# Performance work log

Measured on AMD Instinct MI355X. Metric: run time of the kernel, lower is better.

## Reference

```python
import jax, jax.numpy as jnp
import numpy as np

# Dimensions (production-scale, see shape_source)
B, L, D = 16, 64, 256      # batch, text length, char_emb
U = 500                    # number of distinct units (characters/phonemes)
V = 10000                  # vocab size
MIN_WL, MAX_WL = 4, 10     # min/max extracted word length
WL = MAX_WL - MIN_WL + 1   # number of candidate word lengths (7)
TEMP = 0.1                 # g.temperature
INS_COST = 1.0             # per-character insertion/deletion cost


def setup_inputs() -> dict:
    key = jax.random.key(0)
    k1, k2, k3, k4 = jax.random.split(key, 4)
    word_repr = jax.random.normal(k1, (B, L, D), jnp.float32)
    unit_repr = jax.random.normal(k2, (U, D), jnp.float32)
    indexed_segments = jax.random.randint(k3, (V, MAX_WL), 0, U)
    vocab_length = jax.random.randint(k4, (V,), MIN_WL, MAX_WL + 1)
    return {
        "word_repr": word_repr,
        "unit_repr": unit_repr,
        "indexed_segments": indexed_segments,
        "vocab_length": vocab_length,
    }


def _soft_max(x, axis):
    w = jnp.exp(jax.nn.log_softmax(x / TEMP, axis=axis))
    value = (x * w).sum(axis)
    index = jnp.argmax(x, axis=axis)
    return value, index


def _soft_min(x, axis):
    w = jnp.exp(jax.nn.log_softmax(-x / TEMP, axis=axis))
    value = (x * w).sum(axis)
    index = jnp.argmin(x, axis=axis)
    return value, index


def _soft_threshold(x):
    return (jax.nn.celu(1.0 - 2.0 * x) + 1.0) / 2.0


def reference(word_repr, unit_repr, indexed_segments, vocab_length):
    # --- cosine char-similarity between text positions and vocab units ---
    wn = word_repr / jnp.linalg.norm(word_repr, axis=-1, keepdims=True)   # (B,L,D)
    un = unit_repr / jnp.linalg.norm(unit_repr, axis=-1, keepdims=True)   # (U,D)
    sim = jnp.einsum('bld,ud->blu', wn, un)                               # (B,L,U)
    # pad along length so s+j gathers are in-range; padded dist is masked later
    simp = jnp.pad(sim, ((0, 0), (0, MAX_WL), (0, 0)))                    # (B,L+ML,U)

    wls = jnp.arange(MIN_WL, MAX_WL + 1)                                  # (WL,)

    # --- aligned edit-distance accumulation d(v, w) over char positions ---
    # ed[b,s,k,v] = sum_{j < min(wl_k, len_v)} (1 - cos(text[b,s+j], vocab_char[v,j]))
    ed = jnp.zeros((B, L, WL, V), jnp.float32)
    for j in range(MAX_WL):
        d_j = 1.0 - simp[:, j:j + L, :][:, :, indexed_segments[:, j]]     # (B,L,V)
        m_j = (j < jnp.minimum(wls[:, None], vocab_length[None, :]))      # (WL,V)
        ed = ed + d_j[:, :, None, :] * m_j.astype(jnp.float32)[None, None]
    # length-mismatch penalty (insert/delete)
    ed = ed + INS_COST * jnp.abs(wls[:, None] - vocab_length[None, :]).astype(jnp.float32)

    # --- soft-min over vocab: matched_ed_dist / matched_vocab ---
    matched_ed, matched_vocab = _soft_min(ed, axis=-1)                    # (B,L,WL)
    matched_length = vocab_length[matched_vocab]                          # (B,L,WL)
    # soft threshold on per-character distance, then score = thresh * |w|
    matched_thresh = _soft_threshold(matched_ed / wls.astype(jnp.float32))
    matched_score = matched_thresh * wls.astype(jnp.float32)              # (B,L,WL)

    # --- viability and scatter restore into dense (batch, len_s, len_e) ---
    s_idx = jnp.arange(L)[:, None]                                        # (L,1)
    viable = (s_idx + wls[None, :]) <= L                                  # (L,WL)
    score = jnp.where(viable[None], matched_score, 0.0)                   # (B,L,WL)
    e_idx = jnp.clip(s_idx + wls[None, :] - 1, 0, L - 1)                  # (L,WL)
    s_grid = jnp.broadcast_to(s_idx, (L, WL))
    dense = jnp.zeros((B, L, L), jnp.float32).at[:, s_grid, e_idx].add(
        score * viable[None].astype(jnp.float32))                         # (B,len_s,len_e)

    # --- soft-max over all candidate spans ---
    flat = dense.reshape(B, L * L)
    best_score, best_idx = _soft_max(flat, axis=-1)                       # (B,)
    start = best_idx // L
    end = best_idx % L
    wl_sel = jnp.clip(end - start + 1 - MIN_WL, 0, WL - 1)
    best_vocab = matched_vocab[jnp.arange(B), start, wl_sel]              # (B,)

    return start, end, best_score, best_vocab, dense
```

## Files before the change

### kernel.cpp

```cpp
#include <hip/hip_runtime.h>

#define NB 16
#define NL 64
#define ND 256
#define NU 500
#define NV 10000
#define MINWL 4
#define MAXWL 10
#define NWL 7
#define ITEMP 10.0f
#define L2I 14.4269504088896f
#define NT 512

__global__ __launch_bounds__(512) void k_sort(const int* __restrict__ vlen,
                                              int* __restrict__ origv,
                                              int* __restrict__ bases) {
    int t = threadIdx.x;
    const int CH = 20;
    int lo = t * CH, hi = min(lo + CH, NV);
    unsigned long long hA = 0, hB = 0;
    for (int v = lo; v < hi; ++v) {
        int l = vlen[v] - MINWL;
        int sh = (l & 3) * 16;
        unsigned long long inc = 1ULL << sh;
        bool isA = l < 4;
        hA += isA ? inc : 0ULL;
        hB += isA ? 0ULL : inc;
    }
    int lane = t & 63, wv = t >> 6;
    unsigned long long iA = hA, iB = hB;
#pragma unroll
    for (int o = 1; o < 64; o <<= 1) {
        unsigned long long a2 = (unsigned long long)__shfl_up((long long)iA, o);
        unsigned long long b2 = (unsigned long long)__shfl_up((long long)iB, o);
        if (lane >= o) { iA += a2; iB += b2; }
    }
    __shared__ unsigned long long wA[8], wB[8];
    __shared__ int base_s[8];
    if (lane == 63) { wA[wv] = iA; wB[wv] = iB; }
    __syncthreads();
    unsigned long long pA = 0, pB = 0, tA = 0, tB = 0;
#pragma unroll
    for (int w2 = 0; w2 < 8; ++w2) {
        if (w2 < wv) { pA += wA[w2]; pB += wB[w2]; }
        tA += wA[w2]; tB += wB[w2];
    }
    unsigned long long eA = pA + iA - hA, eB = pB + iB - hB;
    if (t == 0) {
        int tot[7] = {(int)(tA & 0xFFFF), (int)((tA >> 16) & 0xFFFF),
                      (int)((tA >> 32) & 0xFFFF), (int)((tA >> 48) & 0xFFFF),
                      (int)(tB & 0xFFFF), (int)((tB >> 16) & 0xFFFF),
                      (int)((tB >> 32) & 0xFFFF)};
        int run = 0;
        for (int l = 0; l < 7; ++l) { base_s[l] = run; bases[l] = run; run += tot[l]; }
        base_s[7] = run; bases[7] = run;
    }
    __syncthreads();
    unsigned long long qA = eA + ((unsigned long long)base_s[0] |
                                  ((unsigned long long)base_s[1] << 16) |
                                  ((unsigned long long)base_s[2] << 32) |
                                  ((unsigned long long)base_s[3] << 48));
    unsigned long long qB = eB + ((unsigned long long)base_s[4] |
                                  ((unsigned long long)base_s[5] << 16) |
                                  ((unsigned long long)base_s[6] << 32));
    for (int v = lo; v < hi; ++v) {
        int l = vlen[v] - MINWL;
        int sh = (l & 3) * 16;
        bool isA = l < 4;
        unsigned long long cur = isA ? qA : qB;
        int pos = (int)((cur >> sh) & 0xFFFF);
        origv[pos] = v;
        unsigned long long inc = 1ULL << sh;
        qA += isA ? inc : 0ULL;
        qB += isA ? 0ULL : inc;
    }
}

__global__ __launch_bounds__(256) void k_gather(const int* __restrict__ origv,
                                                const int* __restrict__ seg,
                                                int* __restrict__ segT) {
    int i = blockIdx.x * 256 + threadIdx.x;
    if (i >= NV) return;
    int v = origv[i];
    const int2* sp = (const int2*)(seg + v * MAXWL);
#pragma unroll
    for (int jj = 0; jj < 5; ++jj) {
        int2 p = sp[jj];
        segT[(2 * jj) * NV + i] = p.x;
        segT[(2 * jj + 1) * NV + i] = p.y;
    }
}

#define SSTR 260
#define SIM_LDS_BYTES ((2 * 32 * SSTR + 64) * 4)

__global__ __launch_bounds__(256) void k_sim(const float* __restrict__ word,
                                             const float* __restrict__ unit,
                                             float* __restrict__ sim) {
    extern __shared__ float lds[];
    float* wt = lds;
    float* ut = lds + 32 * SSTR;
    float* scaleW = lds + 64 * SSTR;
    float* scaleU = scaleW + 32;
    int blk = blockIdx.x;
    int uc = blk & 15, lt = (blk >> 4) & 1, b = blk >> 5;
    int l0 = lt * 32, u0 = uc * 32;
    int t = threadIdx.x;

#pragma unroll
    for (int i = 0; i < 32; ++i)
        wt[i * SSTR + t] = word[(b * NL + l0 + i) * ND + t];
#pragma unroll
    for (int i = 0; i < 32; ++i) {
        int u = u0 + i;
        ut[i * SSTR + t] = (u < NU) ? unit[u * ND + t] : 1.0f;
    }
    __syncthreads();
#pragma unroll
    for (int h = 0; h < 2; ++h) {
        int r = (t >> 4) + h * 16, p = t & 15;
        float sw = 0.f, su = 0.f;
#pragma unroll
        for (int c = 0; c < 16; ++c) {
            float x = wt[r * SSTR + p * 16 + c];
            float y = ut[r * SSTR + p * 16 + c];
            sw += x * x; su += y * y;
        }
#pragma unroll
        for (int o = 1; o < 16; o <<= 1) {
            sw += __shfl_xor(sw, o);
            su += __shfl_xor(su, o);
        }
        if (p == 0) { scaleW[r] = 1.0f / sqrtf(sw); scaleU[r] = 1.0f / sqrtf(su); }
    }
    __syncthreads();

    int lane = t & 15;
    int lp = t >> 4;
    int l = lp * 2;
    const float4* w0p = (const float4*)(wt + l * SSTR);
    const float4* w1p = (const float4*)(wt + (l + 1) * SSTR);
    const float4* x0p = (const float4*)(ut + lane * SSTR);
    const float4* x1p = (const float4*)(ut + (lane + 16) * SSTR);
    float a00 = 0.f, a01 = 0.f, a10 = 0.f, a11 = 0.f;
#pragma unroll 8
    for (int dq = 0; dq < ND / 4; ++dq) {
        float4 w0 = w0p[dq], w1 = w1p[dq], x0 = x0p[dq], x1 = x1p[dq];
        a00 += w0.x * x0.x + w0.y * x0.y + w0.z * x0.z + w0.w * x0.w;
        a01 += w0.x * x1.x + w0.y * x1.y + w0.z * x1.z + w0.w * x1.w;
        a10 += w1.x * x0.x + w1.y * x0.y + w1.z * x0.z + w1.w * x0.w;
        a11 += w1.x * x1.x + w1.y * x1.y + w1.z * x1.z + w1.w * x1.w;
    }
    float sw0 = scaleW[l], sw1 = scaleW[l + 1];
    float su0 = scaleU[lane], su1 = scaleU[lane + 16];
    int gu0 = u0 + lane, gu1 = u0 + lane + 16;
    int base = (b * NL + l0 + l) * NU;
    if (gu0 < NU) { sim[base + gu0] = a00 * (sw0 * su0); sim[base + NU + gu0] = a10 * (sw1 * su0); }
    if (gu1 < NU) { sim[base + gu1] = a01 * (sw0 * su1); sim[base + NU + gu1] = a11 * (sw1 * su1); }
}


template <int CTRL, int RM, bool BC>
__device__ __forceinline__ void red_step(float& m, int& ix, float& S, float& W) {
    float tm = __int_as_float(__builtin_amdgcn_update_dpp(
        __float_as_int(m), __float_as_int(m), CTRL, RM, 0xF, false));
    int ti = __builtin_amdgcn_update_dpp(ix, ix, CTRL, RM, 0xF, false);
    float tS = __int_as_float(__builtin_amdgcn_update_dpp(
        0, __float_as_int(S), CTRL, RM, 0xF, BC));
    float tW = __int_as_float(__builtin_amdgcn_update_dpp(
        0, __float_as_int(W), CTRL, RM, 0xF, BC));
    bool take = (tm < m) || (tm == m && ti < ix);
    ix = take ? ti : ix;
    m = take ? tm : m;
    S += tS;
    W += tW;
}

template <int L>
__device__ __forceinline__ void bucket_pass(int lo, int hi, int t, int wlmax, int kmax,
                                            const int* __restrict__ segT,
                                            const float* __restrict__ dl,
                                            float* m, float* S, float* W, int* ix) {
    if (L - 5 > kmax) return;
    float Sb = 0.f, Wb = 0.f, Sm = 0.f, Wm = 0.f;
    float mb = 3.0e38f, mm = 3.0e38f;
    int ixb = 0, ixm = 0;
    for (int i0 = lo; i0 < hi; i0 += NT) {
        int i = i0 + t;
        bool valid = i < hi;
        int ic = valid ? i : hi - 1;
        float d[L];
#pragma unroll
        for (int j = 0; j < L; ++j) {
            float g = dl[j * NU + segT[j * NV + ic]];
            d[j] = (j < 4) ? g : ((j < wlmax) ? g : 0.0f);
        }
        d[0] = valid ? d[0] : 3.0e38f;
        float q = ((d[0] + d[1]) + d[2]) + d[3];
        float pm = q;
#pragma unroll
        for (int j = 4; j < L; ++j) {
            if (j == L - 1) pm = q;
            q += d[j];
        }
        float wb = __builtin_amdgcn_exp2f(fmaf(q, -L2I, (float)L * L2I));
        Sb += wb;
        Wb = fmaf(q, wb, Wb);
        bool ltb = q < mb;
        ixb = ltb ? i : ixb;
        mb = ltb ? q : mb;
        if constexpr (L >= 5) {
            float edm = pm + 1.0f;
            float wm_ = __builtin_amdgcn_exp2f(fmaf(edm, -L2I, (float)(L - 1) * L2I));
            Sm += wm_;
            Wm = fmaf(edm, wm_, Wm);
            bool ltm = edm < mm;
            ixm = ltm ? i : ixm;
            mm = ltm ? edm : mm;
        }
    }
#pragma unroll
    for (int k = 0; k < NWL; ++k) {
        if (k >= L - 4) {
            if (k <= kmax) {
                float c = (float)(k + 4 - L);
                S[k] += Sb;
                W[k] += fmaf(c, Sb, Wb);
                float cand = mb + c;
                bool take = (cand < m[k]) || (cand == m[k] && ixb < ix[k]);
                ix[k] = take ? ixb : ix[k];
                m[k] = take ? cand : m[k];
            }
        }
        if constexpr (L >= 5) {
            if (k == L - 5 && k <= kmax) {
                S[k] += Sm;
                W[k] += Wm;
                bool take = (mm < m[k]) || (mm == m[k] && ixm < ix[k]);
                ix[k] = take ? ixm : ix[k];
                m[k] = take ? mm : m[k];
            }
        }
    }
}

__global__ __launch_bounds__(NT, 4) void k_extract(const float* __restrict__ sim,
                                                   const int* __restrict__ segT,
                                                   const int* __restrict__ origv,
                                                   const int* __restrict__ basesG,
                                                   float* __restrict__ dense,
                                                   int* __restrict__ mv) {
    int blk = blockIdx.x;
    int s = blk & (NL - 1), b = blk >> 6;
    int t = threadIdx.x;
    int wlmax = min(MAXWL, NL - s);
    if (wlmax < MINWL) {
        if (t < NL) dense[blk * NL + t] = 0.0f;
        return;
    }
    int kmax = wlmax - MINWL;

    int bs[8];
#pragma unroll
    for (int i = 0; i < 8; ++i) bs[i] = __builtin_amdgcn_readfirstlane(basesG[i]);

    __shared__ float dl[MAXWL * NU];
    for (int j = 0; j < wlmax; ++j)
        if (t < NU) dl[j * NU + t] = 1.0f - sim[(b * NL + s + j) * NU + t];
    __syncthreads();

    float m[NWL], S[NWL], W[NWL];
    int ix[NWL];
#pragma unroll
    for (int k = 0; k < NWL; ++k) { m[k] = 3.0e38f; S[k] = 0.f; W[k] = 0.f; ix[k] = 0; }

    bucket_pass<4>(bs[0], bs[1], t, wlmax, kmax, segT, dl, m, S, W, ix);
    bucket_pass<5>(bs[1], bs[2], t, wlmax, kmax, segT, dl, m, S, W, ix);
    bucket_pass<6>(bs[2], bs[3], t, wlmax, kmax, segT, dl, m, S, W, ix);
    bucket_pass<7>(bs[3], bs[4], t, wlmax, kmax, segT, dl, m, S, W, ix);
    bucket_pass<8>(bs[4], bs[5], t, wlmax, kmax, segT, dl, m, S, W, ix);
    bucket_pass<9>(bs[5], bs[6], t, wlmax, kmax, segT, dl, m, S, W, ix);
    bucket_pass<10>(bs[6], bs[7], t, wlmax, kmax, segT, dl, m, S, W, ix);

#pragma unroll
    for (int k = 0; k < NWL; ++k) {
        red_step<0x111, 0xF, true>(m[k], ix[k], S[k], W[k]);
        red_step<0x112, 0xF, true>(m[k], ix[k], S[k], W[k]);
        red_step<0x114, 0xF, true>(m[k], ix[k], S[k], W[k]);
        red_step<0x118, 0xF, true>(m[k], ix[k], S[k], W[k]);
        red_step<0x142, 0xA, false>(m[k], ix[k], S[k], W[k]);
        red_step<0x143, 0xC, false>(m[k], ix[k], S[k], W[k]);
    }

    __syncthreads();
    float* rm = dl;
    float* rS = dl + 64;
    float* rW = dl + 128;
    int* rI = (int*)(dl + 192);
    float* scoreRow = dl + 256;
    int wv = t >> 6;
    if ((t & 63) == 63) {
#pragma unroll
        for (int k = 0; k < NWL; ++k) {
            rm[wv * NWL + k] = m[k]; rS[wv * NWL + k] = S[k];
            rW[wv * NWL + k] = W[k]; rI[wv * NWL + k] = ix[k];
        }
    }
    __syncthreads();
    if (t < NWL) {
        int k = t;
        float mm = rm[k], SS = rS[k], WW = rW[k];
        int II = rI[k];
#pragma unroll
        for (int w2 = 1; w2 < 8; ++w2) {
            float m2 = rm[w2 * NWL + k];
            int i2 = rI[w2 * NWL + k];
            bool take = (m2 < mm) || (m2 == mm && i2 < II);
            II = take ? i2 : II;
            mm = take ? m2 : mm;
            SS += rS[w2 * NWL + k];
            WW += rW[w2 * NWL + k];
        }
        if (k <= kmax) {
            float med = WW / SS;
            float wl = (float)(MINWL + k);
            float z = 1.0f - 2.0f * (med / wl);
            float cel = (z > 0.f) ? z : (__expf(z) - 1.0f);
            scoreRow[k] = 0.5f * (cel + 1.0f) * wl;
            mv[(b * NL + s) * NWL + k] = origv[II];
        }
    }
    __syncthreads();
    if (t < NL) {
        int k = t - s - (MINWL - 1);
        float val = (k >= 0 && k <= kmax) ? scoreRow[k] : 0.0f;
        dense[blk * NL + t] = val;
    }
}

__global__ __launch_bounds__(256) void k_final(const float* __restrict__ dense,
                                               const int* __restrict__ mv,
                                               float* __restrict__ out) {
    int b = blockIdx.x, t = threadIdx.x;
    float m = -3.0e38f, S = 0.f, W = 0.f;
    int ix = 0;
    for (int i = t; i < NL * NL; i += 256) {
        float x = dense[b * NL * NL + i];
        if (x > m) {
            float f = __expf((m - x) * ITEMP);
            S = S * f + 1.0f;
            W = W * f + x;
            m = x;
            ix = i;
        } else {
            float w = __expf((x - m) * ITEMP);
            S += w;
            W += x * w;
        }
    }
#pragma unroll
    for (int o = 32; o >= 1; o >>= 1) {
        float m2 = __shfl_down(m, o);
        float S2 = __shfl_down(S, o);
        float W2 = __shfl_down(W, o);
        int i2 = __shfl_down(ix, o);
        float mx = fmaxf(m, m2);
        float fa = __expf((m - mx) * ITEMP);
        float fb = __expf((m2 - mx) * ITEMP);
        S = S * fa + S2 * fb;
        W = W * fa + W2 * fb;
        ix = (m2 > m || (m2 == m && i2 < ix)) ? i2 : ix;
        m = mx;
    }
    __shared__ float rm[4], rS[4], rW[4];
    __shared__ int rI[4];
    if ((t & 63) == 0) { int wv = t >> 6; rm[wv] = m; rS[wv] = S; rW[wv] = W; rI[wv] = ix; }
    __syncthreads();
    if (t == 0) {
        float mm = rm[0], SS = rS[0], WW = rW[0];
        int II = rI[0];
#pragma unroll
        for (int wv = 1; wv < 4; ++wv) {
            float m2 = rm[wv], S2 = rS[wv], W2 = rW[wv];
            int i2 = rI[wv];
            float mx = fmaxf(mm, m2);
            float fa = __expf((mm - mx) * ITEMP);
            float fb = __expf((m2 - mx) * ITEMP);
            SS = SS * fa + S2 * fb;
            WW = WW * fa + W2 * fb;
            II = (m2 > mm || (m2 == mm && i2 < II)) ? i2 : II;
            mm = mx;
        }
        float best = WW / SS;
        int st = II >> 6, en = II & (NL - 1);
        int ks = en - st + 1 - MINWL;
        ks = ks < 0 ? 0 : (ks > NWL - 1 ? NWL - 1 : ks);
        int bv = mv[(b * NL + st) * NWL + ks];
        out[b] = (float)st;
        out[NB + b] = (float)en;
        out[2 * NB + b] = best;
        out[3 * NB + b] = (float)bv;
    }
}

extern "C" void kernel_launch(void* const* d_in, const int* in_sizes, int n_in,
                              void* d_out, int out_size, void* d_ws, size_t ws_size,
                              hipStream_t stream) {
    const float* word = (const float*)d_in[0];
    const float* unit = (const float*)d_in[1];
    const int* seg = (const int*)d_in[2];
    const int* vlen = (const int*)d_in[3];
    float* out = (float*)d_out;
    char* ws = (char*)d_ws;
    float* sim = (float*)ws;
    int* mv = (int*)(ws + 2048000);
    int* origv = (int*)(ws + 2076672);
    int* segT = (int*)(ws + 2116672);
    int* bases = (int*)(ws + 2516672);
    float* dense = out + 4 * NB;

    hipFuncSetAttribute((const void*)k_sim,
                        hipFuncAttributeMaxDynamicSharedMemorySize, SIM_LDS_BYTES);

    k_sort<<<1, 512, 0, stream>>>(vlen, origv, bases);
    k_gather<<<(NV + 255) / 256, 256, 0, stream>>>(origv, seg, segT);
    k_sim<<<NB * 2 * 16, 256, SIM_LDS_BYTES, stream>>>(word, unit, sim);
    k_extract<<<NB * NL, NT, 0, stream>>>(sim, segT, origv, bases, dense, mv);
    k_final<<<NB, 256, 0, stream>>>(dense, mv, out);
}
```

Before: 72.06 us.

## Parallelize extract over vocab chunks with lanes mapped to start positions

The extract kernel previously ran one block per (batch, start) and had threads stride over the vocab. Now each block holds one batch's full distance table (74 padded rows) in LDS and handles one vocab chunk. Each lane takes one start position and walks a contiguous vocab sub-range, so all lanes in a wave read the same segment indices (a broadcast load) while indexing different LDS rows. Partial softmin stats go to workspace and a new merge kernel combines them, computes scores, writes dense output and does the final soft-max. The final soft-max uses a closed-form count for the zero entries. The costs are large LDS use per block, an extra partial-result pass and LDS bank conflicts from the row stride.

```diff
diff --git a/kernel.cpp b/kernel.cpp
--- a/kernel.cpp
+++ b/kernel.cpp
@@ -11,6 +11,12 @@
 #define ITEMP 10.0f
 #define L2I 14.4269504088896f
 #define NT 512
+#define NCH 16
+#define ROWS 74
+#define RSTR 501
+#define SEGP 12
+#define NSK (NWL * 64)
+#define NZERO 3690.0f
 
 __global__ __launch_bounds__(512) void k_sort(const int* __restrict__ vlen,
                                               int* __restrict__ origv,
@@ -78,17 +84,16 @@
 
 __global__ __launch_bounds__(256) void k_gather(const int* __restrict__ origv,
                                                 const int* __restrict__ seg,
-                                                int* __restrict__ segT) {
+                                                int* __restrict__ segS) {
     int i = blockIdx.x * 256 + threadIdx.x;
     if (i >= NV) return;
     int v = origv[i];
     const int2* sp = (const int2*)(seg + v * MAXWL);
-#pragma unroll
-    for (int jj = 0; jj < 5; ++jj) {
-        int2 p = sp[jj];
-        segT[(2 * jj) * NV + i] = p.x;
-        segT[(2 * jj + 1) * NV + i] = p.y;
-    }
+    int2 p0 = sp[0], p1 = sp[1], p2 = sp[2], p3 = sp[3], p4 = sp[4];
+    int4* dst = (int4*)(segS + i * SEGP);
+    dst[0] = make_int4(p0.x, p0.y, p1.x, p1.y);
+    dst[1] = make_int4(p2.x, p2.y, p3.x, p3.y);
+    dst[2] = make_int4(p4.x, p4.y, 0, 0);
 }
 
 #define SSTR 260
@@ -160,80 +165,67 @@
 }
 
 
-template <int CTRL, int RM, bool BC>
-__device__ __forceinline__ void red_step(float& m, int& ix, float& S, float& W) {
-    float tm = __int_as_float(__builtin_amdgcn_update_dpp(
-        __float_as_int(m), __float_as_int(m), CTRL, RM, 0xF, false));
-    int ti = __builtin_amdgcn_update_dpp(ix, ix, CTRL, RM, 0xF, false);
-    float tS = __int_as_float(__builtin_amdgcn_update_dpp(
-        0, __float_as_int(S), CTRL, RM, 0xF, BC));
-    float tW = __int_as_float(__builtin_amdgcn_update_dpp(
-        0, __float_as_int(W), CTRL, RM, 0xF, BC));
-    bool take = (tm < m) || (tm == m && ti < ix);
-    ix = take ? ti : ix;
-    m = take ? tm : m;
-    S += tS;
-    W += tW;
-}
-
 template <int L>
-__device__ __forceinline__ void bucket_pass(int lo, int hi, int t, int wlmax, int kmax,
-                                            const int* __restrict__ segT,
-                                            const float* __restrict__ dl,
-                                            float* m, float* S, float* W, int* ix) {
-    if (L - 5 > kmax) return;
-    float Sb = 0.f, Wb = 0.f, Sm = 0.f, Wm = 0.f;
-    float mb = 3.0e38f, mm = 3.0e38f;
+__device__ __forceinline__ void bucket_passT(int a, int bnd,
+                                             const int* __restrict__ segS,
+                                             const float* __restrict__ dls,
+                                             float* m, float* S, float* W, int* ix) {
+    if (a >= bnd) return;
+    constexpr int NLD = (L + 3) / 4;
+    float Sb = 0.f, Wb = 0.f, mb = 3.0e38f;
+    float Sm = 0.f, Wm = 0.f, mm = 3.0e38f;
     int ixb = 0, ixm = 0;
-    for (int i0 = lo; i0 < hi; i0 += NT) {
-        int i = i0 + t;
-        bool valid = i < hi;
-        int ic = valid ? i : hi - 1;
-        float d[L];
-#pragma unroll
-        for (int j = 0; j < L; ++j) {
-            float g = dl[j * NU + segT[j * NV + ic]];
-            d[j] = (j < 4) ? g : ((j < wlmax) ? g : 0.0f);
-        }
-        d[0] = valid ? d[0] : 3.0e38f;
-        float q = ((d[0] + d[1]) + d[2]) + d[3];
+    const int4* sp = (const int4*)segS;
+    int4 c0 = {}, c1 = {}, c2 = {};
+    c0 = sp[a * 3];
+    if constexpr (NLD > 1) c1 = sp[a * 3 + 1];
+    if constexpr (NLD > 2) c2 = sp[a * 3 + 2];
+    for (int i = a; i < bnd; ++i) {
+        int ip = min(i + 1, bnd - 1);
+        int4 n0 = sp[ip * 3], n1 = {}, n2 = {};
+        if constexpr (NLD > 1) n1 = sp[ip * 3 + 1];
+        if constexpr (NLD > 2) n2 = sp[ip * 3 + 2];
+        int c[10] = {c0.x, c0.y, c0.z, c0.w, c1.x, c1.y, c1.z, c1.w, c2.x, c2.y};
+        float q = ((dls[c[0]] + dls[RSTR + c[1]]) + dls[2 * RSTR + c[2]]) +
+                  dls[3 * RSTR + c[3]];
         float pm = q;
 #pragma unroll
         for (int j = 4; j < L; ++j) {
             if (j == L - 1) pm = q;
-            q += d[j];
+            q += dls[j * RSTR + c[j]];
         }
         float wb = __builtin_amdgcn_exp2f(fmaf(q, -L2I, (float)L * L2I));
         Sb += wb;
         Wb = fmaf(q, wb, Wb);
-        bool ltb = q < mb;
-        ixb = ltb ? i : ixb;
-        mb = ltb ? q : mb;
+        bool lb = q < mb;
+        ixb = lb ? i : ixb;
+        mb = lb ? q : mb;
         if constexpr (L >= 5) {
             float edm = pm + 1.0f;
-            float wm_ = __builtin_amdgcn_exp2f(fmaf(edm, -L2I, (float)(L - 1) * L2I));
-            Sm += wm_;
-            Wm = fmaf(edm, wm_, Wm);
-            bool ltm = edm < mm;
-            ixm = ltm ? i : ixm;
-            mm = ltm ? edm : mm;
-        }
+            float wm = __builtin_amdgcn_exp2f(fmaf(edm, -L2I, (float)(L - 1) * L2I));
+            Sm += wm;
+            Wm = fmaf(edm, wm, Wm);
+            bool lm = edm < mm;
+            ixm = lm ? i : ixm;
+            mm = lm ? edm : mm;
+        }
+        c0 = n0;
+        if constexpr (NLD > 1) c1 = n1;
+        if constexpr (NLD > 2) c2 = n2;
     }
 #pragma unroll
     for (int k = 0; k < NWL; ++k) {
         if (k >= L - 4) {
-            if (k <= kmax) {
-                float c = (float)(k + 4 - L);
-                S[k] += Sb;
-                W[k] += fmaf(c, Sb, Wb);
-                float cand = mb + c;
-                bool take = (cand < m[k]) || (cand == m[k] && ixb < ix[k]);
-                ix[k] = take ? ixb : ix[k];
-                m[k] = take ? cand : m[k];
-            }
+            float c = (float)(k + 4 - L);
+            S[k] += Sb;
+            W[k] += fmaf(c, Sb, Wb);
+            float cand = mb + c;
+            bool take = (cand < m[k]) || (cand == m[k] && ixb < ix[k]);
+            ix[k] = take ? ixb : ix[k];
+            m[k] = take ? cand : m[k];
         }
         if constexpr (L >= 5) {
-            if (k == L - 5 && k <= kmax) {
+            if (k == L - 5) {
                 S[k] += Sm;
                 W[k] += Wm;
                 bool take = (mm < m[k]) || (mm == m[k] && ixm < ix[k]);
@@ -244,162 +236,194 @@
     }
 }
 
-__global__ __launch_bounds__(NT, 4) void k_extract(const float* __restrict__ sim,
-                                                   const int* __restrict__ segT,
-                                                   const int* __restrict__ origv,
-                                                   const int* __restrict__ basesG,
-                                                   float* __restrict__ dense,
-                                                   int* __restrict__ mv) {
+#define EXT_LDS_BYTES (ROWS * RSTR * 4)
+
+__global__ __launch_bounds__(NT) void k_extract(const float* __restrict__ sim,
+                                                const int* __restrict__ segS,
+                                                const int* __restrict__ basesG,
+                                                float* __restrict__ pM,
+                                                float* __restrict__ pS,
+                                                float* __restrict__ pW,
+                                                int* __restrict__ pI) {
+    extern __shared__ float dl[];
     int blk = blockIdx.x;
-    int s = blk & (NL - 1), b = blk >> 6;
+    int ch = blk & (NCH - 1), b = blk >> 4;
     int t = threadIdx.x;
-    int wlmax = min(MAXWL, NL - s);
-    if (wlmax < MINWL) {
-        if (t < NL) dense[blk * NL + t] = 0.0f;
-        return;
-    }
-    int kmax = wlmax - MINWL;
+    int s = t & 63, w = t >> 6;
+
+    for (int r = 0; r < ROWS; ++r)
+        for (int u = t; u < NU; u += NT)
+            dl[r * RSTR + u] = (r < NL) ? (1.0f - sim[(b * NL + r) * NU + u]) : 0.0f;
+    __syncthreads();
 
     int bs[8];
 #pragma unroll
-    for (int i = 0; i < 8; ++i) bs[i] = __builtin_amdgcn_readfirstlane(basesG[i]);
-
-    __shared__ float dl[MAXWL * NU];
-    for (int j = 0; j < wlmax; ++j)
-        if (t < NU) dl[j * NU + t] = 1.0f - sim[(b * NL + s + j) * NU + t];
-    __syncthreads();
+    for (int i = 0; i < 8; ++i) bs[i] = basesG[i];
 
     float m[NWL], S[NWL], W[NWL];
     int ix[NWL];
 #pragma unroll
     for (int k = 0; k < NWL; ++k) { m[k] = 3.0e38f; S[k] = 0.f; W[k] = 0.f; ix[k] = 0; }
 
-    bucket_pass<4>(bs[0], bs[1], t, wlmax, kmax, segT, dl, m, S, W, ix);
-    bucket_pass<5>(bs[1], bs[2], t, wlmax, kmax, segT, dl, m, S, W, ix);
-    bucket_pass<6>(bs[2], bs[3], t, wlmax, kmax, segT, dl, m, S, W, ix);
-    bucket_pass<7>(bs[3], bs[4], t, wlmax, kmax, segT, dl, m, S, W, ix);
-    bucket_pass<8>(bs[4], bs[5], t, wlmax, kmax, segT, dl, m, S, W, ix);
-    bucket_pass<9>(bs[5], bs[6], t, wlmax, kmax, segT, dl, m, S, W, ix);
-    bucket_pass<10>(bs[6], bs[7], t, wlmax, kmax, segT, dl, m, S, W, ix);
-
+    const float* dls = dl + s * RSTR;
+
+    int a[7], e[7];
+#pragma unroll
+    for (int l = 0; l < 7; ++l) {
+        int lo = bs[l], hi = bs[l + 1];
+        int n = hi - lo;
+        int pc = (n + NCH - 1) >> 4;
+        int cs = lo + ch * pc;
+        int ce = min(cs + pc, hi);
+        int n2 = max(ce - cs, 0);
+        int pw = (n2 + 7) >> 3;
+        a[l] = cs + w * pw;
+        e[l] = min(a[l] + pw, ce);
+    }
+    bucket_passT<4>(a[0], e[0], segS, dls, m, S, W, ix);
+    bucket_passT<5>(a[1], e[1], segS, dls, m, S, W, ix);
+    bucket_passT<6>(a[2], e[2], segS, dls, m, S, W, ix);
+    bucket_passT<7>(a[3], e[3], segS, dls, m, S, W, ix);
+    bucket_passT<8>(a[4], e[4], segS, dls, m, S, W, ix);
+    bucket_passT<9>(a[5], e[5], segS, dls, m, S, W, ix);
+    bucket_passT<10>(a[6], e[6], segS, dls, m, S, W, ix);
+
+    __syncthreads();
+    float* scrM = dl;
+    float* scrS = dl + 8 * NSK;
+    float* scrW = dl + 16 * NSK;
+    int* scrI = (int*)(dl + 24 * NSK);
 #pragma unroll
     for (int k = 0; k < NWL; ++k) {
-        red_step<0x111, 0xF, true>(m[k], ix[k], S[k], W[k]);
-        red_step<0x112, 0xF, true>(m[k], ix[k], S[k], W[k]);
-        red_step<0x114, 0xF, true>(m[k], ix[k], S[k], W[k]);
-        red_step<0x118, 0xF, true>(m[k], ix[k], S[k], W[k]);
-        red_step<0x142, 0xA, false>(m[k], ix[k], S[k], W[k]);
-        red_step<0x143, 0xC, false>(m[k], ix[k], S[k], W[k]);
-    }
-
-    __syncthreads();
-    float* rm = dl;
-    float* rS = dl + 64;
-    float* rW = dl + 128;
-    int* rI = (int*)(dl + 192);
-    float* scoreRow = dl + 256;
-    int wv = t >> 6;
-    if ((t & 63) == 63) {
-#pragma unroll
-        for (int k = 0; k < NWL; ++k) {
-            rm[wv * NWL + k] = m[k]; rS[wv * NWL + k] = S[k];
-            rW[wv * NWL + k] = W[k]; rI[wv * NWL + k] = ix[k];
-        }
-    }
-    __syncthreads();
-    if (t < NWL) {
-        int k = t;
-        float mm = rm[k], SS = rS[k], WW = rW[k];
-        int II = rI[k];
+        int o = (w * NWL + k) * 64 + s;
+        scrM[o] = m[k]; scrS[o] = S[k]; scrW[o] = W[k]; scrI[o] = ix[k];
+    }
+    __syncthreads();
+    if (t < NSK) {
+        int k = t >> 6, ss = t & 63;
+        int o0 = k * 64 + ss;
+        float mm = scrM[o0], SS = scrS[o0], WW = scrW[o0];
+        int II = scrI[o0];
 #pragma unroll
         for (int w2 = 1; w2 < 8; ++w2) {
-            float m2 = rm[w2 * NWL + k];
-            int i2 = rI[w2 * NWL + k];
+            int o = (w2 * NWL + k) * 64 + ss;
+            float m2 = scrM[o];
+            int i2 = scrI[o];
             bool take = (m2 < mm) || (m2 == mm && i2 < II);
             II = take ? i2 : II;
             mm = take ? m2 : mm;
-            SS += rS[w2 * NWL + k];
-            WW += rW[w2 * NWL + k];
-        }
+            SS += scrS[o];
+            WW += scrW[o];
+        }
+        int off = (b * NCH + ch) * NSK + t;
+        pM[off] = mm; pS[off] = SS; pW[off] = WW; pI[off] = II;
+    }
+}
+
+__global__ __launch_bounds__(NT) void k_merge(const float* __restrict__ pM,
+                                              const float* __restrict__ pS,
+                                              const float* __restrict__ pW,
+                                              const int* __restrict__ pI,
+                                              const int* __restrict__ origv,
+                                              float* __restrict__ out) {
+    int b = blockIdx.x, t = threadIdx.x;
+    __shared__ float score[NSK];
+    __shared__ int ixf[NSK];
+    __shared__ float rm[8], rS[8], rW[8];
+    __shared__ int rX[8];
+    __shared__ float gm;
+    __shared__ int gfl;
+
+    float x = -1.0f;
+    int fl = 0x7FFFFFFF;
+    if (t < NSK) {
+        int base = b * NCH * NSK + t;
+        float mm = pM[base], SS = pS[base], WW = pW[base];
+        int II = pI[base];
+        for (int c = 1; c < NCH; ++c) {
+            int o = base + c * NSK;
+            float m2 = pM[o];
+            int i2 = pI[o];
+            bool take = (m2 < mm) || (m2 == mm && i2 < II);
+            II = take ? i2 : II;
+            mm = take ? m2 : mm;
+            SS += pS[o];
+            WW += pW[o];
+        }
+        int k = t >> 6, ss = t & 63;
+        int kmax = min(NWL - 1, 60 - ss);
         if (k <= kmax) {
             float med = WW / SS;
             float wl = (float)(MINWL + k);
             float z = 1.0f - 2.0f * (med / wl);
             float cel = (z > 0.f) ? z : (__expf(z) - 1.0f);
-            scoreRow[k] = 0.5f * (cel + 1.0f) * wl;
-            mv[(b * NL + s) * NWL + k] = origv[II];
-        }
-    }
-    __syncthreads();
-    if (t < NL) {
-        int k = t - s - (MINWL - 1);
-        float val = (k >= 0 && k <= kmax) ? scoreRow[k] : 0.0f;
-        dense[blk * NL + t] = val;
-    }
-}
-
-__global__ __launch_bounds__(256) void k_final(const float* __restrict__ dense,
-                                               const int* __restrict__ mv,
-                                               float* __restrict__ out) {
-    int b = blockIdx.x, t = threadIdx.x;
-    float m = -3.0e38f, S = 0.f, W = 0.f;
-    int ix = 0;
-    for (int i = t; i < NL * NL; i += 256) {
-        float x = dense[b * NL * NL + i];
-        if (x > m) {
-            float f = __expf((m - x) * ITEMP);
-            S = S * f + 1.0f;
-            W = W * f + x;
-            m = x;
-            ix = i;
-        } else {
-            float w = __expf((x - m) * ITEMP);
-            S += w;
-            W += x * w;
-        }
-    }
+            x = 0.5f * (cel + 1.0f) * wl;
+            ixf[t] = II;
+            fl = ss * 64 + (ss + k + 3);
+        }
+        score[t] = (k <= kmax) ? x : 0.0f;
+    }
+    __syncthreads();
+
+    float mv = x;
+    int mf = fl;
 #pragma unroll
     for (int o = 32; o >= 1; o >>= 1) {
-        float m2 = __shfl_down(m, o);
-        float S2 = __shfl_down(S, o);
-        float W2 = __shfl_down(W, o);
-        int i2 = __shfl_down(ix, o);
-        float mx = fmaxf(m, m2);
-        float fa = __expf((m - mx) * ITEMP);
-        float fb = __expf((m2 - mx) * ITEMP);
-        S = S * fa + S2 * fb;
-        W = W * fa + W2 * fb;
-        ix = (m2 > m || (m2 == m && i2 < ix)) ? i2 : ix;
-        m = mx;
-    }
-    __shared__ float rm[4], rS[4], rW[4];
-    __shared__ int rI[4];
-    if ((t & 63) == 0) { int wv = t >> 6; rm[wv] = m; rS[wv] = S; rW[wv] = W; rI[wv] = ix; }
+        float m2 = __shfl_down(mv, o);
+        int f2 = __shfl_down(mf, o);
+        bool take = (m2 > mv) || (m2 == mv && f2 < mf);
+        mv = take ? m2 : mv;
+        mf = take ? f2 : mf;
+    }
+    if ((t & 63) == 0) { rm[t >> 6] = mv; rX[t >> 6] = mf; }
     __syncthreads();
     if (t == 0) {
-        float mm = rm[0], SS = rS[0], WW = rW[0];
-        int II = rI[0];
-#pragma unroll
-        for (int wv = 1; wv < 4; ++wv) {
-            float m2 = rm[wv], S2 = rS[wv], W2 = rW[wv];
-            int i2 = rI[wv];
-            float mx = fmaxf(mm, m2);
-            float fa = __expf((mm - mx) * ITEMP);
-            float fb = __expf((m2 - mx) * ITEMP);
-            SS = SS * fa + S2 * fb;
-            WW = WW * fa + W2 * fb;
-            II = (m2 > mm || (m2 == mm && i2 < II)) ? i2 : II;
-            mm = mx;
-        }
+        float mm = rm[0];
+        int ff = rX[0];
+#pragma unroll
+        for (int w2 = 1; w2 < 8; ++w2) {
+            bool take = (rm[w2] > mm) || (rm[w2] == mm && rX[w2] < ff);
+            mm = take ? rm[w2] : mm;
+            ff = take ? rX[w2] : ff;
+        }
+        gm = mm; gfl = ff;
+    }
+    __syncthreads();
+    float M = gm;
+
+    float Sl = 0.f, Wl = 0.f;
+    if (x >= 0.0f) {
+        float wq = __expf((x - M) * ITEMP);
+        Sl = wq;
+        Wl = x * wq;
+    }
+#pragma unroll
+    for (int o = 32; o >= 1; o >>= 1) {
+        Sl += __shfl_down(Sl, o);
+        Wl += __shfl_down(Wl, o);
+    }
+    if ((t & 63) == 0) { rS[t >> 6] = Sl; rW[t >> 6] = Wl; }
+    __syncthreads();
+    if (t == 0) {
+        float SS = 0.f, WW = 0.f;
+#pragma unroll
+        for (int w2 = 0; w2 < 8; ++w2) { SS += rS[w2]; WW += rW[w2]; }
+        SS += NZERO * __expf(-M * ITEMP);
         float best = WW / SS;
-        int st = II >> 6, en = II & (NL - 1);
-        int ks = en - st + 1 - MINWL;
-        ks = ks < 0 ? 0 : (ks > NWL - 1 ? NWL - 1 : ks);
-        int bv = mv[(b * NL + st) * NWL + ks];
+        int st = gfl >> 6, en = gfl & 63;
+        int ks = en - st - 3;
+        int II = ixf[ks * 64 + st];
         out[b] = (float)st;
         out[NB + b] = (float)en;
         out[2 * NB + b] = best;
-        out[3 * NB + b] = (float)bv;
+        out[3 * NB + b] = (float)origv[II];
+    }
+
+    float* dense = out + 4 * NB + b * NL * NL;
+    for (int f = t; f < NL * NL; f += NT) {
+        int ss = f >> 6, ee = f & 63;
+        int k = ee - ss - 3;
+        dense[f] = (k >= 0 && k < NWL) ? score[k * 64 + ss] : 0.0f;
     }
 }
 
@@ -413,18 +437,22 @@
     float* out = (float*)d_out;
     char* ws = (char*)d_ws;
     float* sim = (float*)ws;
-    int* mv = (int*)(ws + 2048000);
-    int* origv = (int*)(ws + 2076672);
-    int* segT = (int*)(ws + 2116672);
-    int* bases = (int*)(ws + 2516672);
-    float* dense = out + 4 * NB;
+    int* origv = (int*)(ws + 2048000);
+    int* bases = (int*)(ws + 2088000);
+    int* segS = (int*)(ws + 2088032);
+    float* pM = (float*)(ws + 2568032);
+    float* pS = (float*)(ws + 3026784);
+    float* pW = (float*)(ws + 3485536);
+    int* pI = (int*)(ws + 3944288);
 
     hipFuncSetAttribute((const void*)k_sim,
                         hipFuncAttributeMaxDynamicSharedMemorySize, SIM_LDS_BYTES);
+    hipFuncSetAttribute((const void*)k_extract,
+                        hipFuncAttributeMaxDynamicSharedMemorySize, EXT_LDS_BYTES);
 
     k_sort<<<1, 512, 0, stream>>>(vlen, origv, bases);
-    k_gather<<<(NV + 255) / 256, 256, 0, stream>>>(origv, seg, segT);
+    k_gather<<<(NV + 255) / 256, 256, 0, stream>>>(origv, seg, segS);
     k_sim<<<NB * 2 * 16, 256, SIM_LDS_BYTES, stream>>>(word, unit, sim);
-    k_extract<<<NB * NL, NT, 0, stream>>>(sim, segT, origv, bases, dense, mv);
-    k_final<<<NB, 256, 0, stream>>>(dense, mv, out);
-}
+    k_extract<<<NB * NCH, NT, EXT_LDS_BYTES, stream>>>(sim, segS, bases, pM, pS, pW, pI);
+    k_merge<<<NB, NT, 0, stream>>>(pM, pS, pW, pI, origv, out);
+}
```

Measured after the change: 86.52 us. 20.1% more time.
